# Kernel tuning notes

Measured on AMD Instinct MI355X. Metric: run time of the kernel, lower is better.

Reference implementation:

```python
import jax, jax.numpy as jnp
import numpy as np

SIZES = [(200000, 100000), (100000, 50000), (50000, 25000)]  # (n_src, n_dst) per layer
E = [1600000, 800000, 400000]
IN_C, HID, OUT_C = 128, 256, 47
BN_EPS = 1e-5


def setup_inputs() -> dict:
    key = jax.random.key(0)
    ks = jax.random.split(key, 32)
    inp = {"x": jax.random.normal(ks[0], (SIZES[0][0], IN_C), jnp.float32)}
    for i in range(3):
        inp[f"row{i}"] = jax.random.randint(ks[1 + 2 * i], (E[i],), 0, SIZES[i][0], dtype=jnp.int32)
        inp[f"col{i}"] = jax.random.randint(ks[2 + 2 * i], (E[i],), 0, SIZES[i][1], dtype=jnp.int32)
    dims = [IN_C, HID, HID]
    for i in range(3):
        inp[f"Wl{i}"] = jax.random.normal(ks[10 + 4 * i], (HID, dims[i]), jnp.float32) * 0.05
        inp[f"Wr{i}"] = jax.random.normal(ks[11 + 4 * i], (HID, dims[i]), jnp.float32) * 0.05
        inp[f"g{i}"] = jnp.ones((HID,), jnp.float32)
        inp[f"b{i}"] = jnp.zeros((HID,), jnp.float32)
    inp["Wlin"] = jax.random.normal(ks[25], (OUT_C, 3 * HID), jnp.float32) * 0.05
    inp["blin"] = jnp.zeros((OUT_C,), jnp.float32)
    return inp


def _sage_bn_relu(x_src, row, col, Wl, Wr, g, b, n_dst):
    """Bipartite SAGEConv (mean aggr, bias=False) + BatchNorm(eval) + ReLU."""
    x_dst = x_src[:n_dst]
    msg = x_src[row]                                             # [E, d] gather
    agg = jax.ops.segment_sum(msg, col, num_segments=n_dst)      # scatter-add
    cnt = jax.ops.segment_sum(jnp.ones(row.shape, x_src.dtype), col, num_segments=n_dst)
    agg = agg / jnp.maximum(cnt, 1.0)[:, None]                   # mean over in-neighbors
    h = agg @ Wl.T + x_dst @ Wr.T                                # lin_l + lin_r
    # BatchNorm1d in eval mode with fresh running stats (mean=0, var=1)
    h = h * jax.lax.rsqrt(jnp.asarray(1.0 + BN_EPS, h.dtype)) * g + b
    return jax.nn.relu(h)


def reference(x, row0, col0, row1, col1, row2, col2,
              Wl0, Wr0, g0, b0, Wl1, Wr1, g1, b1, Wl2, Wr2, g2, b2,
              Wlin, blin):
    rows = (row0, row1, row2)
    cols = (col0, col1, col2)
    Wls, Wrs = (Wl0, Wl1, Wl2), (Wr0, Wr1, Wr2)
    gs, bs = (g0, g1, g2), (b0, b1, b2)
    end = SIZES[-1][1]  # end_size = adj_t[-1][-1][1]
    h = x
    xs = []
    for i in range(3):
        h = _sage_bn_relu(h, rows[i], cols[i], Wls[i], Wrs[i], gs[i], bs[i], SIZES[i][1])
        xs.append(h[:end])
    z = jnp.concatenate(xs, axis=-1) @ Wlin.T + blin  # JK 'cat' + final Linear
    return jax.nn.log_softmax(z, axis=-1)
```

## Files before the change

### kernel.cpp

```cpp
#include <hip/hip_runtime.h>
#include <hip/hip_bf16.h>


#define N_DST0 100000
#define N_DST1 50000
#define N_DST2 25000
#define HID 256
#define OUTC 47
#define ENDR 25000
#define DRC 512
#define NBMAX 256
#define CHUNK 8192
#define BN_SCALE 0.99999500003749969f

#define SEL3(y, a, b, c) ((y) == 0 ? (a) : ((y) == 1 ? (b) : (c)))

typedef __attribute__((ext_vector_type(8))) short short8;
typedef __attribute__((ext_vector_type(4))) float f32x4;

__device__ __forceinline__ unsigned short f2b1(float f) {
    unsigned int u = __float_as_uint(f);
    return (unsigned short)((u + 0x7fffu + ((u >> 16) & 1u)) >> 16);
}
__device__ __forceinline__ float b2f_lo(unsigned int v) {
    return __uint_as_float(v << 16);
}
__device__ __forceinline__ float b2f_hi(unsigned int v) {
    return __uint_as_float(v & 0xffff0000u);
}
__device__ __forceinline__ unsigned int pack2(float lo, float hi) {
    return (unsigned int)f2b1(lo) | ((unsigned int)f2b1(hi) << 16);
}

__global__ __launch_bounds__(256) void f2b_kernel(
    const float* __restrict__ in, unsigned short* __restrict__ out, int n)
{
    int i = (blockIdx.x * 256 + threadIdx.x) * 4;
    if (i < n) {
        float4 v = *(const float4*)&in[i];
        uint2 o;
        o.x = pack2(v.x, v.y);
        o.y = pack2(v.z, v.w);
        *(uint2*)&out[i] = o;
    }
}

__global__ __launch_bounds__(256) void f2b_multi(
    const float* s0, const float* s1, const float* s2, const float* s3,
    const float* s4, const float* s5, const float* s6,
    unsigned short* d0, unsigned short* d1, unsigned short* d2,
    unsigned short* d3, unsigned short* d4, unsigned short* d5,
    unsigned short* d6)
{
    int idx = (blockIdx.x * 256 + threadIdx.x) * 4;
    const float* s; unsigned short* d; int off;
    if (idx < 65536)       { if (idx < 32768)  { s = s0; d = d0; off = 0; }
                             else              { s = s1; d = d1; off = 32768; } }
    else if (idx < 196608) { if (idx < 131072) { s = s2; d = d2; off = 65536; }
                             else              { s = s3; d = d3; off = 131072; } }
    else if (idx < 327680) { if (idx < 262144) { s = s4; d = d4; off = 196608; }
                             else              { s = s5; d = d5; off = 262144; } }
    else if (idx < 363776) { s = s6; d = d6; off = 327680; }
    else return;
    int j = idx - off;
    float4 v = *(const float4*)&s[j];
    uint2 o;
    o.x = pack2(v.x, v.y);
    o.y = pack2(v.z, v.w);
    *(uint2*)&d[j] = o;
}

__global__ __launch_bounds__(256) void bucket_hist_all(
    const int* c0, const int* c1, const int* c2,
    int* __restrict__ bhist, int E0, int E1, int E2)
{
    const int y = blockIdx.y;
    const int* col = SEL3(y, c0, c1, c2);
    const int E = SEL3(y, E0, E1, E2);
    __shared__ int h[NBMAX];
    const int t = threadIdx.x;
    h[t] = 0;
    __syncthreads();
    const int stride = gridDim.x * 256;
    for (int i = blockIdx.x * 256 + t; i < E; i += stride)
        atomicAdd(&h[col[i] >> 9], 1);
    __syncthreads();
    int v = h[t];
    if (v) atomicAdd(&bhist[(y * NBMAX + t) * 16], v);
}

__global__ __launch_bounds__(256) void bucket_scan_all(
    const int* __restrict__ bhist, int* __restrict__ bstart,
    int* __restrict__ bcur)
{
    const int y = blockIdx.x;
    const int t = threadIdx.x;
    __shared__ int sh[256];
    int v = bhist[(y * NBMAX + t) * 16];
    sh[t] = v;
    __syncthreads();
    for (int off = 1; off < 256; off <<= 1) {
        int x = (t >= off) ? sh[t - off] : 0;
        __syncthreads();
        sh[t] += x;
        __syncthreads();
    }
    int ex = sh[t] - v;
    bstart[y * (NBMAX + 1) + t] = ex;
    if (t == 255) bstart[y * (NBMAX + 1) + 256] = sh[255];
    bcur[y * NBMAX * 16 + t * 16] = ex;
}

__global__ __launch_bounds__(256) void multisplit_all(
    const int* r0, const int* r1, const int* r2,
    const int* c0, const int* c1, const int* c2,
    int* bcur, unsigned int* p0, unsigned int* p1, unsigned int* p2,
    int E0, int E1, int E2)
{
    const int y = blockIdx.y;
    const int E = SEL3(y, E0, E1, E2);
    const int base = blockIdx.x * CHUNK;
    if (base >= E) return;
    const int* row = SEL3(y, r0, r1, r2);
    const int* col = SEL3(y, c0, c1, c2);
    int* bc = bcur + y * (NBMAX * 16);
    unsigned int* part = SEL3(y, p0, p1, p2);

    __shared__ int hist[NBMAX];
    __shared__ int segoff[NBMAX + 1];
    __shared__ int cur[NBMAX];
    __shared__ int delta[NBMAX];
    __shared__ unsigned int stage[CHUNK];
    __shared__ unsigned char bstage[CHUNK];

    const int t = threadIdx.x;
    const int n = min(CHUNK, E - base);

    hist[t] = 0;
    __syncthreads();
    for (int i = t; i < n; i += 256)
        atomicAdd(&hist[col[base + i] >> 9], 1);
    __syncthreads();

    int v = hist[t];
    cur[t] = v;
    __syncthreads();
    for (int off = 1; off < 256; off <<= 1) {
        int x = (t >= off) ? cur[t - off] : 0;
        __syncthreads();
        cur[t] += x;
        __syncthreads();
    }
    segoff[t + 1] = cur[t];
    if (t == 0) segoff[0] = 0;
    __syncthreads();
    int so = segoff[t];
    cur[t] = so;
    if (v > 0) {
        int g = atomicAdd(&bc[t * 16], v);
        delta[t] = g - so;
    }
    __syncthreads();

    for (int i = t; i < n; i += 256) {
        int c = col[base + i];
        int r = row[base + i];
        int b = c >> 9;
        int p = atomicAdd(&cur[b], 1);
        stage[p] = ((unsigned)(c & 511) << 18) | (unsigned)r;
        bstage[p] = (unsigned char)b;
    }
    __syncthreads();

    for (int i = t; i < n; i += 256) {
        int b = bstage[i];
        part[delta[b] + i] = stage[i];
    }
}

__global__ __launch_bounds__(256) void bucket_csr_all(
    const unsigned int* p0, const unsigned int* p1, const unsigned int* p2,
    const int* __restrict__ bstart,
    int* g0, int* g1, int* g2, int* x0, int* x1, int* x2,
    int* s0, int* s1, int* s2, int n0, int n1, int n2)
{
    const int y = blockIdx.y;
    const int n_dst = SEL3(y, n0, n1, n2);
    const int b = blockIdx.x;
    const int d0 = b * DRC;
    if (d0 >= n_dst) return;
    const unsigned int* part = SEL3(y, p0, p1, p2);
    const int* bs = bstart + y * (NBMAX + 1);
    int* deg  = SEL3(y, g0, g1, g2);
    int* excl = SEL3(y, x0, x1, x2);
    int* esrc = SEL3(y, s0, s1, s2);

    __shared__ int h[DRC];
    __shared__ int cur2[DRC];
    __shared__ int tsum[256];
    const int t = threadIdx.x;
    h[t] = 0; h[t + 256] = 0;
    __syncthreads();
    const int wstart = bs[b], wend = bs[b + 1];
    for (int i = wstart + t; i < wend; i += 256)
        atomicAdd(&h[part[i] >> 18], 1);
    __syncthreads();

    int h0 = h[2 * t], h1 = h[2 * t + 1];
    int ps = h0 + h1;
    tsum[t] = ps;
    __syncthreads();
    for (int off = 1; off < 256; off <<= 1) {
        int x = (t >= off) ? tsum[t - off] : 0;
        __syncthreads();
        tsum[t] += x;
        __syncthreads();
    }
    int exp_ = tsum[t] - ps;
    cur2[2 * t]     = wstart + exp_;
    cur2[2 * t + 1] = wstart + exp_ + h0;
    __syncthreads();

    for (int j = t; j < DRC; j += 256) {
        int d = d0 + j;
        if (d < n_dst) { deg[d] = h[j]; excl[d] = cur2[j]; }
    }
    __syncthreads();

    for (int i = wstart + t; i < wend; i += 256) {
        unsigned int v = part[i];
        int pos = atomicAdd(&cur2[v >> 18], 1);
        esrc[pos] = (int)(v & 0x3FFFFu);
    }
}

template<int LOGK>
__global__ __launch_bounds__(256) void gather_mean(
    const unsigned short* __restrict__ xsrc, const int* __restrict__ esrc,
    const int* __restrict__ start, const int* __restrict__ deg,
    unsigned short* __restrict__ agg, int n_dst)
{
    const int wid = (blockIdx.x * 256 + threadIdx.x) >> 6;
    const int lane = threadIdx.x & 63;
    if (wid >= n_dst) return;
    const int sub = lane >> 5;
    const int cl  = lane & 31;
    const int s = start[wid];
    const int d = deg[wid];
    const float inv = 1.0f / (float)max(d, 1);

    if (LOGK == 7) {
        float a0 = 0, a1 = 0, a2 = 0, a3 = 0;
        const size_t coff = (size_t)cl * 4;
        int i = 0;
        for (; i + 8 <= d; i += 8) {
            int e0 = esrc[s + i + 0 + sub], e1 = esrc[s + i + 2 + sub];
            int e2 = esrc[s + i + 4 + sub], e3 = esrc[s + i + 6 + sub];
            uint2 v0 = *(const uint2*)&xsrc[((size_t)e0 << 7) + coff];
            uint2 v1 = *(const uint2*)&xsrc[((size_t)e1 << 7) + coff];
            uint2 v2 = *(const uint2*)&xsrc[((size_t)e2 << 7) + coff];
            uint2 v3 = *(const uint2*)&xsrc[((size_t)e3 << 7) + coff];
            a0 += b2f_lo(v0.x) + b2f_lo(v1.x) + b2f_lo(v2.x) + b2f_lo(v3.x);
            a1 += b2f_hi(v0.x) + b2f_hi(v1.x) + b2f_hi(v2.x) + b2f_hi(v3.x);
            a2 += b2f_lo(v0.y) + b2f_lo(v1.y) + b2f_lo(v2.y) + b2f_lo(v3.y);
            a3 += b2f_hi(v0.y) + b2f_hi(v1.y) + b2f_hi(v2.y) + b2f_hi(v3.y);
        }
        for (; i + 2 <= d; i += 2) {
            int e0 = esrc[s + i + sub];
            uint2 v0 = *(const uint2*)&xsrc[((size_t)e0 << 7) + coff];
            a0 += b2f_lo(v0.x); a1 += b2f_hi(v0.x);
            a2 += b2f_lo(v0.y); a3 += b2f_hi(v0.y);
        }
        if (i < d && sub == 0) {
            int e0 = esrc[s + i];
            uint2 v0 = *(const uint2*)&xsrc[((size_t)e0 << 7) + coff];
            a0 += b2f_lo(v0.x); a1 += b2f_hi(v0.x);
            a2 += b2f_lo(v0.y); a3 += b2f_hi(v0.y);
        }
        a0 += __shfl_xor(a0, 32); a1 += __shfl_xor(a1, 32);
        a2 += __shfl_xor(a2, 32); a3 += __shfl_xor(a3, 32);
        if (sub == 0) {
            uint2 o;
            o.x = pack2(a0 * inv, a1 * inv);
            o.y = pack2(a2 * inv, a3 * inv);
            *(uint2*)&agg[((size_t)wid << 7) + coff] = o;
        }
    } else {
        float a0 = 0, a1 = 0, a2 = 0, a3 = 0, a4 = 0, a5 = 0, a6 = 0, a7 = 0;
        const size_t coff = (size_t)cl * 8;
        int i = 0;
        for (; i + 8 <= d; i += 8) {
            int e0 = esrc[s + i + 0 + sub], e1 = esrc[s + i + 2 + sub];
            int e2 = esrc[s + i + 4 + sub], e3 = esrc[s + i + 6 + sub];
            uint4 v0 = *(const uint4*)&xsrc[((size_t)e0 << 8) + coff];
            uint4 v1 = *(const uint4*)&xsrc[((size_t)e1 << 8) + coff];
            uint4 v2 = *(const uint4*)&xsrc[((size_t)e2 << 8) + coff];
            uint4 v3 = *(const uint4*)&xsrc[((size_t)e3 << 8) + coff];
            a0 += b2f_lo(v0.x) + b2f_lo(v1.x) + b2f_lo(v2.x) + b2f_lo(v3.x);
            a1 += b2f_hi(v0.x) + b2f_hi(v1.x) + b2f_hi(v2.x) + b2f_hi(v3.x);
            a2 += b2f_lo(v0.y) + b2f_lo(v1.y) + b2f_lo(v2.y) + b2f_lo(v3.y);
            a3 += b2f_hi(v0.y) + b2f_hi(v1.y) + b2f_hi(v2.y) + b2f_hi(v3.y);
            a4 += b2f_lo(v0.z) + b2f_lo(v1.z) + b2f_lo(v2.z) + b2f_lo(v3.z);
            a5 += b2f_hi(v0.z) + b2f_hi(v1.z) + b2f_hi(v2.z) + b2f_hi(v3.z);
            a6 += b2f_lo(v0.w) + b2f_lo(v1.w) + b2f_lo(v2.w) + b2f_lo(v3.w);
            a7 += b2f_hi(v0.w) + b2f_hi(v1.w) + b2f_hi(v2.w) + b2f_hi(v3.w);
        }
        for (; i + 2 <= d; i += 2) {
            int e0 = esrc[s + i + sub];
            uint4 v0 = *(const uint4*)&xsrc[((size_t)e0 << 8) + coff];
            a0 += b2f_lo(v0.x); a1 += b2f_hi(v0.x);
            a2 += b2f_lo(v0.y); a3 += b2f_hi(v0.y);
            a4 += b2f_lo(v0.z); a5 += b2f_hi(v0.z);
            a6 += b2f_lo(v0.w); a7 += b2f_hi(v0.w);
        }
        if (i < d && sub == 0) {
            int e0 = esrc[s + i];
            uint4 v0 = *(const uint4*)&xsrc[((size_t)e0 << 8) + coff];
            a0 += b2f_lo(v0.x); a1 += b2f_hi(v0.x);
            a2 += b2f_lo(v0.y); a3 += b2f_hi(v0.y);
            a4 += b2f_lo(v0.z); a5 += b2f_hi(v0.z);
            a6 += b2f_lo(v0.w); a7 += b2f_hi(v0.w);
        }
        a0 += __shfl_xor(a0, 32); a1 += __shfl_xor(a1, 32);
        a2 += __shfl_xor(a2, 32); a3 += __shfl_xor(a3, 32);
        a4 += __shfl_xor(a4, 32); a5 += __shfl_xor(a5, 32);
        a6 += __shfl_xor(a6, 32); a7 += __shfl_xor(a7, 32);
        if (sub == 0) {
            uint4 o;
            o.x = pack2(a0 * inv, a1 * inv);
            o.y = pack2(a2 * inv, a3 * inv);
            o.z = pack2(a4 * inv, a5 * inv);
            o.w = pack2(a6 * inv, a7 * inv);
            *(uint4*)&agg[((size_t)wid << 8) + coff] = o;
        }
    }
}

template<int KH>
__global__ __launch_bounds__(512) void sage_gemm_mfma(
    const unsigned short* __restrict__ aggb, const unsigned short* __restrict__ xdstb,
    const unsigned short* __restrict__ Wlb, const unsigned short* __restrict__ Wrb,
    const float* __restrict__ g, const float* __restrict__ b,
    unsigned short* __restrict__ h, int n_dst)
{
    __shared__ uint4 A_sh[512];
    __shared__ uint4 B_sh[1024];

    const int tid  = threadIdx.x;
    const int lane = tid & 63;
    const int wv   = tid >> 6;
    const int mh   = wv >> 2;
    const int n0   = (wv & 3) * 64;
    const int m0g  = blockIdx.x * 128;
    const int lrow = lane & 15;
    const int lgrp = lane >> 4;

    f32x4 acc[4][4];
#pragma unroll
    for (int i = 0; i < 4; ++i)
#pragma unroll
        for (int j = 0; j < 4; ++j)
            acc[i][j] = (f32x4){0.f, 0.f, 0.f, 0.f};

    for (int kp = 0; kp < 2 * KH; kp += 32) {
        const unsigned short* Asrc = (kp < KH) ? aggb : xdstb;
        const unsigned short* Bsrc = (kp < KH) ? Wlb : Wrb;
        const int kbase = (kp < KH) ? kp : kp - KH;

        {
            int m = tid >> 2, gq = tid & 3;
            int r = m0g + m;
            uint4 v = {0, 0, 0, 0};
            if (r < n_dst) v = *(const uint4*)&Asrc[(size_t)r * KH + kbase + gq * 8];
            A_sh[m * 4 + (gq ^ ((m >> 1) & 3))] = v;
        }
        {
            int nb_ = tid >> 2, gq = tid & 3;
#pragma unroll
            for (int i2 = 0; i2 < 2; ++i2) {
                int n = nb_ + 128 * i2;
                uint4 v = *(const uint4*)&Bsrc[(size_t)n * KH + kbase + gq * 8];
                B_sh[n * 4 + (gq ^ ((n >> 1) & 3))] = v;
            }
        }
        __syncthreads();

        short8 av[4], bv[4];
#pragma unroll
        for (int mf = 0; mf < 4; ++mf) {
            int m = mh * 64 + mf * 16 + lrow;
            av[mf] = *reinterpret_cast<const short8*>(&A_sh[m * 4 + (lgrp ^ ((m >> 1) & 3))]);
        }
#pragma unroll
        for (int nf = 0; nf < 4; ++nf) {
            int n = n0 + nf * 16 + lrow;
            bv[nf] = *reinterpret_cast<const short8*>(&B_sh[n * 4 + (lgrp ^ ((n >> 1) & 3))]);
        }
#pragma unroll
        for (int mf = 0; mf < 4; ++mf)
#pragma unroll
            for (int nf = 0; nf < 4; ++nf)
                acc[mf][nf] = __builtin_amdgcn_mfma_f32_16x16x32_bf16(
                    av[mf], bv[nf], acc[mf][nf], 0, 0, 0);
        __syncthreads();
    }

#pragma unroll
    for (int nf = 0; nf < 4; ++nf) {
        int n = n0 + nf * 16 + lrow;
        float sc = g[n] * BN_SCALE;
        float bi = b[n];
#pragma unroll
        for (int mf = 0; mf < 4; ++mf) {
            int mbase = m0g + mh * 64 + mf * 16 + lgrp * 4;
#pragma unroll
            for (int r = 0; r < 4; ++r) {
                int m = mbase + r;
                if (m < n_dst) {
                    float vv = fmaxf(acc[mf][nf][r] * sc + bi, 0.f);
                    h[(size_t)m * HID + n] = f2b1(vv);
                }
            }
        }
    }
}

__global__ __launch_bounds__(256) void final_mfma(
    const unsigned short* __restrict__ h0, const unsigned short* __restrict__ h1,
    const unsigned short* __restrict__ h2, const unsigned short* __restrict__ wlinb,
    const float* __restrict__ blin, float* __restrict__ out)
{
    __shared__ uint4 A_sh[512];
    __shared__ uint4 B_sh[256];

    const int tid  = threadIdx.x;
    const int lane = tid & 63;
    const int wv   = tid >> 6;
    const int m0g  = blockIdx.x * 128;
    const int lrow = lane & 15;
    const int lgrp = lane >> 4;

    f32x4 acc[2][4];
#pragma unroll
    for (int i = 0; i < 2; ++i)
#pragma unroll
        for (int j = 0; j < 4; ++j)
            acc[i][j] = (f32x4){0.f, 0.f, 0.f, 0.f};

    for (int kp = 0; kp < 768; kp += 32) {
        const int seg = kp >> 8;
        const unsigned short* hs = (seg == 0) ? h0 : (seg == 1) ? h1 : h2;
        const int kseg = kp & 255;

#pragma unroll
        for (int l = 0; l < 2; ++l) {
            int idx = tid + l * 256;
            int m = idx >> 2, gq = idx & 3;
            int r = m0g + m;
            uint4 v = {0, 0, 0, 0};
            if (r < ENDR) v = *(const uint4*)&hs[(size_t)r * HID + kseg + gq * 8];
            A_sh[m * 4 + (gq ^ ((m >> 1) & 3))] = v;
        }
        {
            int n = tid >> 2, gq = tid & 3;
            uint4 v = *(const uint4*)&wlinb[(size_t)n * 768 + kp + gq * 8];
            B_sh[n * 4 + (gq ^ ((n >> 1) & 3))] = v;
        }
        __syncthreads();

        short8 av[2], bv[4];
#pragma unroll
        for (int mf = 0; mf < 2; ++mf) {
            int m = wv * 32 + mf * 16 + lrow;
            av[mf] = *reinterpret_cast<const short8*>(&A_sh[m * 4 + (lgrp ^ ((m >> 1) & 3))]);
        }
#pragma unroll
        for (int nf = 0; nf < 4; ++nf) {
            int n = nf * 16 + lrow;
            bv[nf] = *reinterpret_cast<const short8*>(&B_sh[n * 4 + (lgrp ^ ((n >> 1) & 3))]);
        }
#pragma unroll
        for (int mf = 0; mf < 2; ++mf)
#pragma unroll
            for (int nf = 0; nf < 4; ++nf)
                acc[mf][nf] = __builtin_amdgcn_mfma_f32_16x16x32_bf16(
                    av[mf], bv[nf], acc[mf][nf], 0, 0, 0);
        __syncthreads();
    }

    float bv4[4];
#pragma unroll
    for (int nf = 0; nf < 4; ++nf) {
        int n = nf * 16 + lrow;
        bv4[nf] = (n < OUTC) ? blin[n] : 0.f;
    }

#pragma unroll
    for (int mf = 0; mf < 2; ++mf) {
        float z[4][4];
        float rmax[4], rsum[4];
#pragma unroll
        for (int r = 0; r < 4; ++r) {
            float mx = -INFINITY;
#pragma unroll
            for (int nf = 0; nf < 4; ++nf) {
                int n = nf * 16 + lrow;
                float v = (n < OUTC) ? acc[mf][nf][r] + bv4[nf] : -INFINITY;
                z[r][nf] = v;
                mx = fmaxf(mx, v);
            }
            rmax[r] = mx;
        }
#pragma unroll
        for (int off = 8; off >= 1; off >>= 1)
#pragma unroll
            for (int r = 0; r < 4; ++r)
                rmax[r] = fmaxf(rmax[r], __shfl_xor(rmax[r], off));
#pragma unroll
        for (int r = 0; r < 4; ++r) {
            float s = 0.f;
#pragma unroll
            for (int nf = 0; nf < 4; ++nf)
                s += (z[r][nf] > -INFINITY) ? expf(z[r][nf] - rmax[r]) : 0.f;
            rsum[r] = s;
        }
#pragma unroll
        for (int off = 8; off >= 1; off >>= 1)
#pragma unroll
            for (int r = 0; r < 4; ++r)
                rsum[r] += __shfl_xor(rsum[r], off);

#pragma unroll
        for (int r = 0; r < 4; ++r) {
            int m = m0g + wv * 32 + mf * 16 + lgrp * 4 + r;
            if (m < ENDR) {
                float lg = rmax[r] + logf(rsum[r]);
#pragma unroll
                for (int nf = 0; nf < 4; ++nf) {
                    int n = nf * 16 + lrow;
                    if (n < OUTC) out[(size_t)m * OUTC + n] = z[r][nf] - lg;
                }
            }
        }
    }
}

extern "C" void kernel_launch(void* const* d_in, const int* in_sizes, int n_in,
                              void* d_out, int out_size, void* d_ws, size_t ws_size,
                              hipStream_t stream)
{
    const float* x    = (const float*)d_in[0];
    const int* rows[3] = {(const int*)d_in[1], (const int*)d_in[3], (const int*)d_in[5]};
    const int* cols[3] = {(const int*)d_in[2], (const int*)d_in[4], (const int*)d_in[6]};
    const float* Wl[3] = {(const float*)d_in[7],  (const float*)d_in[11], (const float*)d_in[15]};
    const float* Wr[3] = {(const float*)d_in[8],  (const float*)d_in[12], (const float*)d_in[16]};
    const float* gs[3] = {(const float*)d_in[9],  (const float*)d_in[13], (const float*)d_in[17]};
    const float* bs[3] = {(const float*)d_in[10], (const float*)d_in[14], (const float*)d_in[18]};
    const float* Wlin = (const float*)d_in[19];
    const float* blin = (const float*)d_in[20];
    float* out = (float*)d_out;

    const int E0 = in_sizes[1], E1 = in_sizes[3], E2 = in_sizes[5];

    char* base = (char*)d_ws;
    unsigned short* xb   = (unsigned short*)(base);
    unsigned short* h0b  = (unsigned short*)(base + 51200000);
    unsigned short* h1b  = (unsigned short*)(base + 102400000);
    unsigned short* h2b  = (unsigned short*)(base + 128000000);
    unsigned short* aggb = (unsigned short*)(base + 140800000);
    unsigned short* wb   = (unsigned short*)(base + 166400000);
    unsigned short* wlinb= (unsigned short*)(base + 167100032);
    int* ibase = (int*)(base + 167600000);
    int* esrc0 = ibase;
    int* esrc1 = ibase + 1600000;
    int* esrc2 = ibase + 2400000;
    int* deg0  = ibase + 2800000;
    int* deg1  = ibase + 2900000;
    int* deg2  = ibase + 2950000;
    int* excl0 = ibase + 3000000;
    int* excl1 = ibase + 3100000;
    int* excl2 = ibase + 3150000;
    int* bcur  = ibase + 3200000;
    int* bhist = ibase + 3220000;
    int* bstart= ibase + 3240000;
    unsigned int* part0 = (unsigned int*)(base + 181000000);
    unsigned int* part1 = (unsigned int*)(base + 188000000);
    unsigned int* part2 = (unsigned int*)(base + 192000000);

    unsigned short* Wlb[3] = {wb,          wb + 65536,  wb + 196608};
    unsigned short* Wrb[3] = {wb + 32768,  wb + 131072, wb + 262144};

    f2b_kernel<<<(25600000 / 4 + 255) / 256, 256, 0, stream>>>(x, xb, 25600000);
    hipMemsetAsync(wlinb, 0, 64 * 768 * sizeof(unsigned short), stream);
    f2b_multi<<<356, 256, 0, stream>>>(
        Wl[0], Wr[0], Wl[1], Wr[1], Wl[2], Wr[2], Wlin,
        Wlb[0], Wrb[0], Wlb[1], Wrb[1], Wlb[2], Wrb[2], wlinb);

    hipMemsetAsync(bhist, 0, 3 * NBMAX * 16 * sizeof(int), stream);
    {
        dim3 gh(128, 3);
        bucket_hist_all<<<gh, 256, 0, stream>>>(
            cols[0], cols[1], cols[2], bhist, E0, E1, E2);
        bucket_scan_all<<<3, 256, 0, stream>>>(bhist, bstart, bcur);
        dim3 gms((E0 + CHUNK - 1) / CHUNK, 3);
        multisplit_all<<<gms, 256, 0, stream>>>(
            rows[0], rows[1], rows[2], cols[0], cols[1], cols[2],
            bcur, part0, part1, part2, E0, E1, E2);
        dim3 gbc((N_DST0 + DRC - 1) / DRC, 3);
        bucket_csr_all<<<gbc, 256, 0, stream>>>(
            part0, part1, part2, bstart,
            deg0, deg1, deg2, excl0, excl1, excl2,
            esrc0, esrc1, esrc2, N_DST0, N_DST1, N_DST2);
    }

    const unsigned short* hsrc[3] = {xb, h0b, h1b};
    unsigned short* hdst[3] = {h0b, h1b, h2b};
    int* esrcs[3] = {esrc0, esrc1, esrc2};
    int* excls[3] = {excl0, excl1, excl2};
    int* degs[3]  = {deg0, deg1, deg2};
    const int ndst[3] = {N_DST0, N_DST1, N_DST2};

    for (int L = 0; L < 3; ++L) {
        const int nd = ndst[L];
        if (L == 0) {
            gather_mean<7><<<(nd + 3) / 4, 256, 0, stream>>>(
                hsrc[L], esrcs[L], excls[L], degs[L], aggb, nd);
            sage_gemm_mfma<128><<<(nd + 127) / 128, 512, 0, stream>>>(
                aggb, hsrc[L], Wlb[L], Wrb[L], gs[L], bs[L], hdst[L], nd);
        } else {
            gather_mean<8><<<(nd + 3) / 4, 256, 0, stream>>>(
                hsrc[L], esrcs[L], excls[L], degs[L], aggb, nd);
            sage_gemm_mfma<256><<<(nd + 127) / 128, 512, 0, stream>>>(
                aggb, hsrc[L], Wlb[L], Wrb[L], gs[L], bs[L], hdst[L], nd);
        }
    }

    final_mfma<<<(ENDR + 127) / 128, 256, 0, stream>>>(
        h0b, h1b, h2b, wlinb, blin, out);
}
```

Baseline: 406.1 us.

## Switch intermediates to fp16 with packed-half gather and LDS-staged GEMM epilogue

Replaces bf16 storage and MFMA with fp16 throughout, which lets the gather accumulate with packed half-precision vector adds instead of per-element bf16-to-float unpacking. The layer-0 gather now uses 16-byte loads with four edge groups per wave. The GEMM epilogue stages the output tile in shared memory so rows are written to global memory as coalesced 16-byte stores instead of scattered 2-byte stores. Accumulating in fp16 risks precision loss and overflow for high-degree nodes.

Result: faster. 372.9 us (-8.2%).

```diff
diff --git a/kernel.cpp b/kernel.cpp
--- a/kernel.cpp
+++ b/kernel.cpp
@@ -15,45 +15,37 @@
 
 #define SEL3(y, a, b, c) ((y) == 0 ? (a) : ((y) == 1 ? (b) : (c)))
 
-typedef __attribute__((ext_vector_type(8))) short short8;
+typedef _Float16 f16x8 __attribute__((ext_vector_type(8)));
+typedef _Float16 f16x4 __attribute__((ext_vector_type(4)));
 typedef __attribute__((ext_vector_type(4))) float f32x4;
 
-__device__ __forceinline__ unsigned short f2b1(float f) {
-    unsigned int u = __float_as_uint(f);
-    return (unsigned short)((u + 0x7fffu + ((u >> 16) & 1u)) >> 16);
-}
-__device__ __forceinline__ float b2f_lo(unsigned int v) {
-    return __uint_as_float(v << 16);
-}
-__device__ __forceinline__ float b2f_hi(unsigned int v) {
-    return __uint_as_float(v & 0xffff0000u);
-}
-__device__ __forceinline__ unsigned int pack2(float lo, float hi) {
-    return (unsigned int)f2b1(lo) | ((unsigned int)f2b1(hi) << 16);
-}
-
-__global__ __launch_bounds__(256) void f2b_kernel(
-    const float* __restrict__ in, unsigned short* __restrict__ out, int n)
+__device__ __forceinline__ f16x8 hshfl_add(f16x8 a, int m) {
+    union { f16x8 h; int i[4]; } u, v;
+    u.h = a;
+#pragma unroll
+    for (int j = 0; j < 4; ++j) v.i[j] = __shfl_xor(u.i[j], m);
+    return a + v.h;
+}
+
+__global__ __launch_bounds__(256) void f2h_kernel(
+    const float* __restrict__ in, _Float16* __restrict__ out, int n)
 {
     int i = (blockIdx.x * 256 + threadIdx.x) * 4;
     if (i < n) {
         float4 v = *(const float4*)&in[i];
-        uint2 o;
-        o.x = pack2(v.x, v.y);
-        o.y = pack2(v.z, v.w);
-        *(uint2*)&out[i] = o;
-    }
-}
-
-__global__ __launch_bounds__(256) void f2b_multi(
+        f16x4 o = {(_Float16)v.x, (_Float16)v.y, (_Float16)v.z, (_Float16)v.w};
+        *(f16x4*)&out[i] = o;
+    }
+}
+
+__global__ __launch_bounds__(256) void f2h_multi(
     const float* s0, const float* s1, const float* s2, const float* s3,
     const float* s4, const float* s5, const float* s6,
-    unsigned short* d0, unsigned short* d1, unsigned short* d2,
-    unsigned short* d3, unsigned short* d4, unsigned short* d5,
-    unsigned short* d6)
+    _Float16* d0, _Float16* d1, _Float16* d2, _Float16* d3,
+    _Float16* d4, _Float16* d5, _Float16* d6)
 {
     int idx = (blockIdx.x * 256 + threadIdx.x) * 4;
-    const float* s; unsigned short* d; int off;
+    const float* s; _Float16* d; int off;
     if (idx < 65536)       { if (idx < 32768)  { s = s0; d = d0; off = 0; }
                              else              { s = s1; d = d1; off = 32768; } }
     else if (idx < 196608) { if (idx < 131072) { s = s2; d = d2; off = 65536; }
@@ -64,10 +56,8 @@
     else return;
     int j = idx - off;
     float4 v = *(const float4*)&s[j];
-    uint2 o;
-    o.x = pack2(v.x, v.y);
-    o.y = pack2(v.z, v.w);
-    *(uint2*)&d[j] = o;
+    f16x4 o = {(_Float16)v.x, (_Float16)v.y, (_Float16)v.z, (_Float16)v.w};
+    *(f16x4*)&d[j] = o;
 }
 
 __global__ __launch_bounds__(256) void bucket_hist_all(
@@ -236,115 +226,88 @@
 
 template<int LOGK>
 __global__ __launch_bounds__(256) void gather_mean(
-    const unsigned short* __restrict__ xsrc, const int* __restrict__ esrc,
+    const _Float16* __restrict__ xsrc, const int* __restrict__ esrc,
     const int* __restrict__ start, const int* __restrict__ deg,
-    unsigned short* __restrict__ agg, int n_dst)
+    _Float16* __restrict__ agg, int n_dst)
 {
     const int wid = (blockIdx.x * 256 + threadIdx.x) >> 6;
     const int lane = threadIdx.x & 63;
     if (wid >= n_dst) return;
-    const int sub = lane >> 5;
-    const int cl  = lane & 31;
     const int s = start[wid];
     const int d = deg[wid];
     const float inv = 1.0f / (float)max(d, 1);
+    f16x8 acc = {0, 0, 0, 0, 0, 0, 0, 0};
 
     if (LOGK == 7) {
-        float a0 = 0, a1 = 0, a2 = 0, a3 = 0;
-        const size_t coff = (size_t)cl * 4;
-        int i = 0;
-        for (; i + 8 <= d; i += 8) {
-            int e0 = esrc[s + i + 0 + sub], e1 = esrc[s + i + 2 + sub];
-            int e2 = esrc[s + i + 4 + sub], e3 = esrc[s + i + 6 + sub];
-            uint2 v0 = *(const uint2*)&xsrc[((size_t)e0 << 7) + coff];
-            uint2 v1 = *(const uint2*)&xsrc[((size_t)e1 << 7) + coff];
-            uint2 v2 = *(const uint2*)&xsrc[((size_t)e2 << 7) + coff];
-            uint2 v3 = *(const uint2*)&xsrc[((size_t)e3 << 7) + coff];
-            a0 += b2f_lo(v0.x) + b2f_lo(v1.x) + b2f_lo(v2.x) + b2f_lo(v3.x);
-            a1 += b2f_hi(v0.x) + b2f_hi(v1.x) + b2f_hi(v2.x) + b2f_hi(v3.x);
-            a2 += b2f_lo(v0.y) + b2f_lo(v1.y) + b2f_lo(v2.y) + b2f_lo(v3.y);
-            a3 += b2f_hi(v0.y) + b2f_hi(v1.y) + b2f_hi(v2.y) + b2f_hi(v3.y);
-        }
-        for (; i + 2 <= d; i += 2) {
-            int e0 = esrc[s + i + sub];
-            uint2 v0 = *(const uint2*)&xsrc[((size_t)e0 << 7) + coff];
-            a0 += b2f_lo(v0.x); a1 += b2f_hi(v0.x);
-            a2 += b2f_lo(v0.y); a3 += b2f_hi(v0.y);
-        }
-        if (i < d && sub == 0) {
-            int e0 = esrc[s + i];
-            uint2 v0 = *(const uint2*)&xsrc[((size_t)e0 << 7) + coff];
-            a0 += b2f_lo(v0.x); a1 += b2f_hi(v0.x);
-            a2 += b2f_lo(v0.y); a3 += b2f_hi(v0.y);
-        }
-        a0 += __shfl_xor(a0, 32); a1 += __shfl_xor(a1, 32);
-        a2 += __shfl_xor(a2, 32); a3 += __shfl_xor(a3, 32);
-        if (sub == 0) {
-            uint2 o;
-            o.x = pack2(a0 * inv, a1 * inv);
-            o.y = pack2(a2 * inv, a3 * inv);
-            *(uint2*)&agg[((size_t)wid << 7) + coff] = o;
-        }
-    } else {
-        float a0 = 0, a1 = 0, a2 = 0, a3 = 0, a4 = 0, a5 = 0, a6 = 0, a7 = 0;
+        const int sub = lane >> 4;
+        const int cl  = lane & 15;
         const size_t coff = (size_t)cl * 8;
         int i = 0;
         for (; i + 8 <= d; i += 8) {
-            int e0 = esrc[s + i + 0 + sub], e1 = esrc[s + i + 2 + sub];
+            int e0 = esrc[s + i + sub], e1 = esrc[s + i + 4 + sub];
+            f16x8 v0 = *(const f16x8*)&xsrc[((size_t)e0 << 7) + coff];
+            f16x8 v1 = *(const f16x8*)&xsrc[((size_t)e1 << 7) + coff];
+            acc += v0;
+            acc += v1;
+        }
+        for (; i + 4 <= d; i += 4) {
+            int e0 = esrc[s + i + sub];
+            acc += *(const f16x8*)&xsrc[((size_t)e0 << 7) + coff];
+        }
+        if (i + sub < d) {
+            int e0 = esrc[s + i + sub];
+            acc += *(const f16x8*)&xsrc[((size_t)e0 << 7) + coff];
+        }
+        acc = hshfl_add(acc, 16);
+        acc = hshfl_add(acc, 32);
+        if (sub == 0) {
+            f16x8 o;
+#pragma unroll
+            for (int j = 0; j < 8; ++j) o[j] = (_Float16)((float)acc[j] * inv);
+            *(f16x8*)&agg[((size_t)wid << 7) + coff] = o;
+        }
+    } else {
+        const int sub = lane >> 5;
+        const int cl  = lane & 31;
+        const size_t coff = (size_t)cl * 8;
+        int i = 0;
+        for (; i + 8 <= d; i += 8) {
+            int e0 = esrc[s + i + sub],     e1 = esrc[s + i + 2 + sub];
             int e2 = esrc[s + i + 4 + sub], e3 = esrc[s + i + 6 + sub];
-            uint4 v0 = *(const uint4*)&xsrc[((size_t)e0 << 8) + coff];
-            uint4 v1 = *(const uint4*)&xsrc[((size_t)e1 << 8) + coff];
-            uint4 v2 = *(const uint4*)&xsrc[((size_t)e2 << 8) + coff];
-            uint4 v3 = *(const uint4*)&xsrc[((size_t)e3 << 8) + coff];
-            a0 += b2f_lo(v0.x) + b2f_lo(v1.x) + b2f_lo(v2.x) + b2f_lo(v3.x);
-            a1 += b2f_hi(v0.x) + b2f_hi(v1.x) + b2f_hi(v2.x) + b2f_hi(v3.x);
-            a2 += b2f_lo(v0.y) + b2f_lo(v1.y) + b2f_lo(v2.y) + b2f_lo(v3.y);
-            a3 += b2f_hi(v0.y) + b2f_hi(v1.y) + b2f_hi(v2.y) + b2f_hi(v3.y);
-            a4 += b2f_lo(v0.z) + b2f_lo(v1.z) + b2f_lo(v2.z) + b2f_lo(v3.z);
-            a5 += b2f_hi(v0.z) + b2f_hi(v1.z) + b2f_hi(v2.z) + b2f_hi(v3.z);
-            a6 += b2f_lo(v0.w) + b2f_lo(v1.w) + b2f_lo(v2.w) + b2f_lo(v3.w);
-            a7 += b2f_hi(v0.w) + b2f_hi(v1.w) + b2f_hi(v2.w) + b2f_hi(v3.w);
+            f16x8 v0 = *(const f16x8*)&xsrc[((size_t)e0 << 8) + coff];
+            f16x8 v1 = *(const f16x8*)&xsrc[((size_t)e1 << 8) + coff];
+            f16x8 v2 = *(const f16x8*)&xsrc[((size_t)e2 << 8) + coff];
+            f16x8 v3 = *(const f16x8*)&xsrc[((size_t)e3 << 8) + coff];
+            acc += v0; acc += v1; acc += v2; acc += v3;
         }
         for (; i + 2 <= d; i += 2) {
             int e0 = esrc[s + i + sub];
-            uint4 v0 = *(const uint4*)&xsrc[((size_t)e0 << 8) + coff];
-            a0 += b2f_lo(v0.x); a1 += b2f_hi(v0.x);
-            a2 += b2f_lo(v0.y); a3 += b2f_hi(v0.y);
-            a4 += b2f_lo(v0.z); a5 += b2f_hi(v0.z);
-            a6 += b2f_lo(v0.w); a7 += b2f_hi(v0.w);
-        }
-        if (i < d && sub == 0) {
-            int e0 = esrc[s + i];
-            uint4 v0 = *(const uint4*)&xsrc[((size_t)e0 << 8) + coff];
-            a0 += b2f_lo(v0.x); a1 += b2f_hi(v0.x);
-            a2 += b2f_lo(v0.y); a3 += b2f_hi(v0.y);
-            a4 += b2f_lo(v0.z); a5 += b2f_hi(v0.z);
-            a6 += b2f_lo(v0.w); a7 += b2f_hi(v0.w);
-        }
-        a0 += __shfl_xor(a0, 32); a1 += __shfl_xor(a1, 32);
-        a2 += __shfl_xor(a2, 32); a3 += __shfl_xor(a3, 32);
-        a4 += __shfl_xor(a4, 32); a5 += __shfl_xor(a5, 32);
-        a6 += __shfl_xor(a6, 32); a7 += __shfl_xor(a7, 32);
+            acc += *(const f16x8*)&xsrc[((size_t)e0 << 8) + coff];
+        }
+        if (i + sub < d) {
+            int e0 = esrc[s + i + sub];
+            acc += *(const f16x8*)&xsrc[((size_t)e0 << 8) + coff];
+        }
+        acc = hshfl_add(acc, 32);
         if (sub == 0) {
-            uint4 o;
-            o.x = pack2(a0 * inv, a1 * inv);
-            o.y = pack2(a2 * inv, a3 * inv);
-            o.z = pack2(a4 * inv, a5 * inv);
-            o.w = pack2(a6 * inv, a7 * inv);
-            *(uint4*)&agg[((size_t)wid << 8) + coff] = o;
+            f16x8 o;
+#pragma unroll
+            for (int j = 0; j < 8; ++j) o[j] = (_Float16)((float)acc[j] * inv);
+            *(f16x8*)&agg[((size_t)wid << 8) + coff] = o;
         }
     }
 }
 
 template<int KH>
 __global__ __launch_bounds__(512) void sage_gemm_mfma(
-    const unsigned short* __restrict__ aggb, const unsigned short* __restrict__ xdstb,
-    const unsigned short* __restrict__ Wlb, const unsigned short* __restrict__ Wrb,
+    const _Float16* __restrict__ aggb, const _Float16* __restrict__ xdstb,
+    const _Float16* __restrict__ Wlb, const _Float16* __restrict__ Wrb,
     const float* __restrict__ g, const float* __restrict__ b,
-    unsigned short* __restrict__ h, int n_dst)
-{
-    __shared__ uint4 A_sh[512];
-    __shared__ uint4 B_sh[1024];
+    _Float16* __restrict__ h, int n_dst)
+{
+    __shared__ uint4 SH[2176];
+    uint4* A_sh = SH;
+    uint4* B_sh = SH + 512;
 
     const int tid  = threadIdx.x;
     const int lane = tid & 63;
@@ -363,8 +326,8 @@
             acc[i][j] = (f32x4){0.f, 0.f, 0.f, 0.f};
 
     for (int kp = 0; kp < 2 * KH; kp += 32) {
-        const unsigned short* Asrc = (kp < KH) ? aggb : xdstb;
-        const unsigned short* Bsrc = (kp < KH) ? Wlb : Wrb;
+        const _Float16* Asrc = (kp < KH) ? aggb : xdstb;
+        const _Float16* Bsrc = (kp < KH) ? Wlb : Wrb;
         const int kbase = (kp < KH) ? kp : kp - KH;
 
         {
@@ -385,49 +348,65 @@
         }
         __syncthreads();
 
-        short8 av[4], bv[4];
+        f16x8 av[4], bv[4];
 #pragma unroll
         for (int mf = 0; mf < 4; ++mf) {
             int m = mh * 64 + mf * 16 + lrow;
-            av[mf] = *reinterpret_cast<const short8*>(&A_sh[m * 4 + (lgrp ^ ((m >> 1) & 3))]);
+            av[mf] = *reinterpret_cast<const f16x8*>(&A_sh[m * 4 + (lgrp ^ ((m >> 1) & 3))]);
         }
 #pragma unroll
         for (int nf = 0; nf < 4; ++nf) {
             int n = n0 + nf * 16 + lrow;
-            bv[nf] = *reinterpret_cast<const short8*>(&B_sh[n * 4 + (lgrp ^ ((n >> 1) & 3))]);
+            bv[nf] = *reinterpret_cast<const f16x8*>(&B_sh[n * 4 + (lgrp ^ ((n >> 1) & 3))]);
         }
 #pragma unroll
         for (int mf = 0; mf < 4; ++mf)
 #pragma unroll
             for (int nf = 0; nf < 4; ++nf)
-                acc[mf][nf] = __builtin_amdgcn_mfma_f32_16x16x32_bf16(
+                acc[mf][nf] = __builtin_amdgcn_mfma_f32_16x16x32_f16(
                     av[mf], bv[nf], acc[mf][nf], 0, 0, 0);
         __syncthreads();
     }
 
-#pragma unroll
-    for (int nf = 0; nf < 4; ++nf) {
-        int n = n0 + nf * 16 + lrow;
-        float sc = g[n] * BN_SCALE;
-        float bi = b[n];
-#pragma unroll
-        for (int mf = 0; mf < 4; ++mf) {
-            int mbase = m0g + mh * 64 + mf * 16 + lgrp * 4;
-#pragma unroll
-            for (int r = 0; r < 4; ++r) {
-                int m = mbase + r;
-                if (m < n_dst) {
-                    float vv = fmaxf(acc[mf][nf][r] * sc + bi, 0.f);
-                    h[(size_t)m * HID + n] = f2b1(vv);
+    unsigned short* C_sh = (unsigned short*)SH;
+#pragma unroll
+    for (int half = 0; half < 2; ++half) {
+        __syncthreads();
+        if (mh == half) {
+#pragma unroll
+            for (int nf = 0; nf < 4; ++nf) {
+                int n = n0 + nf * 16 + lrow;
+                float sc = g[n] * BN_SCALE;
+                float bi = b[n];
+#pragma unroll
+                for (int mf = 0; mf < 4; ++mf) {
+                    int mloc = mf * 16 + lgrp * 4;
+#pragma unroll
+                    for (int r = 0; r < 4; ++r) {
+                        float vv = fmaxf(acc[mf][nf][r] * sc + bi, 0.f);
+                        _Float16 hv = (_Float16)vv;
+                        C_sh[(mloc + r) * 264 + n] = *(unsigned short*)&hv;
+                    }
                 }
             }
         }
+        __syncthreads();
+        int mbase = m0g + half * 64;
+#pragma unroll
+        for (int k = 0; k < 4; ++k) {
+            int idx = tid + k * 512;
+            int rr = idx >> 5, cc = idx & 31;
+            int m = mbase + rr;
+            if (m < n_dst)
+                *(uint4*)&h[(size_t)m * HID + cc * 8] =
+                    *(const uint4*)&C_sh[rr * 264 + cc * 8];
+        }
     }
 }
 
 __global__ __launch_bounds__(256) void final_mfma(
-    const unsigned short* __restrict__ h0, const unsigned short* __restrict__ h1,
-    const unsigned short* __restrict__ h2, const unsigned short* __restrict__ wlinb,
+    const _Float16* __restrict__ h0, const _Float16* __restrict__ h1,
+    const _Float16* __restrict__ h2, const _Float16* __restrict__ wlinb,
     const float* __restrict__ blin, float* __restrict__ out)
 {
     __shared__ uint4 A_sh[512];
@@ -449,7 +428,7 @@
 
     for (int kp = 0; kp < 768; kp += 32) {
         const int seg = kp >> 8;
-        const unsigned short* hs = (seg == 0) ? h0 : (seg == 1) ? h1 : h2;
+        const _Float16* hs = (seg == 0) ? h0 : (seg == 1) ? h1 : h2;
         const int kseg = kp & 255;
 
 #pragma unroll
@@ -468,22 +447,22 @@
         }
         __syncthreads();
 
-        short8 av[2], bv[4];
+        f16x8 av[2], bv[4];
 #pragma unroll
         for (int mf = 0; mf < 2; ++mf) {
             int m = wv * 32 + mf * 16 + lrow;
-            av[mf] = *reinterpret_cast<const short8*>(&A_sh[m * 4 + (lgrp ^ ((m >> 1) & 3))]);
+            av[mf] = *reinterpret_cast<const f16x8*>(&A_sh[m * 4 + (lgrp ^ ((m >> 1) & 3))]);
         }
 #pragma unroll
         for (int nf = 0; nf < 4; ++nf) {
             int n = nf * 16 + lrow;
-            bv[nf] = *reinterpret_cast<const short8*>(&B_sh[n * 4 + (lgrp ^ ((n >> 1) & 3))]);
+            bv[nf] = *reinterpret_cast<const f16x8*>(&B_sh[n * 4 + (lgrp ^ ((n >> 1) & 3))]);
         }
 #pragma unroll
         for (int mf = 0; mf < 2; ++mf)
 #pragma unroll
             for (int nf = 0; nf < 4; ++nf)
-                acc[mf][nf] = __builtin_amdgcn_mfma_f32_16x16x32_bf16(
+                acc[mf][nf] = __builtin_amdgcn_mfma_f32_16x16x32_f16(
                     av[mf], bv[nf], acc[mf][nf], 0, 0, 0);
         __syncthreads();
     }
@@ -563,13 +542,13 @@
     const int E0 = in_sizes[1], E1 = in_sizes[3], E2 = in_sizes[5];
 
     char* base = (char*)d_ws;
-    unsigned short* xb   = (unsigned short*)(base);
-    unsigned short* h0b  = (unsigned short*)(base + 51200000);
-    unsigned short* h1b  = (unsigned short*)(base + 102400000);
-    unsigned short* h2b  = (unsigned short*)(base + 128000000);
-    unsigned short* aggb = (unsigned short*)(base + 140800000);
-    unsigned short* wb   = (unsigned short*)(base + 166400000);
-    unsigned short* wlinb= (unsigned short*)(base + 167100032);
+    _Float16* xb   = (_Float16*)(base);
+    _Float16* h0b  = (_Float16*)(base + 51200000);
+    _Float16* h1b  = (_Float16*)(base + 102400000);
+    _Float16* h2b  = (_Float16*)(base + 128000000);
+    _Float16* aggb = (_Float16*)(base + 140800000);
+    _Float16* wb   = (_Float16*)(base + 166400000);
+    _Float16* wlinb= (_Float16*)(base + 167100032);
     int* ibase = (int*)(base + 167600000);
     int* esrc0 = ibase;
     int* esrc1 = ibase + 1600000;
@@ -587,12 +566,12 @@
     unsigned int* part1 = (unsigned int*)(base + 188000000);
     unsigned int* part2 = (unsigned int*)(base + 192000000);
 
-    unsigned short* Wlb[3] = {wb,          wb + 65536,  wb + 196608};
-    unsigned short* Wrb[3] = {wb + 32768,  wb + 131072, wb + 262144};
-
-    f2b_kernel<<<(25600000 / 4 + 255) / 256, 256, 0, stream>>>(x, xb, 25600000);
-    hipMemsetAsync(wlinb, 0, 64 * 768 * sizeof(unsigned short), stream);
-    f2b_multi<<<356, 256, 0, stream>>>(
+    _Float16* Wlb[3] = {wb,          wb + 65536,  wb + 196608};
+    _Float16* Wrb[3] = {wb + 32768,  wb + 131072, wb + 262144};
+
+    f2h_kernel<<<(25600000 / 4 + 255) / 256, 256, 0, stream>>>(x, xb, 25600000);
+    hipMemsetAsync(wlinb, 0, 64 * 768 * sizeof(_Float16), stream);
+    f2h_multi<<<356, 256, 0, stream>>>(
         Wl[0], Wr[0], Wl[1], Wr[1], Wl[2], Wr[2], Wlin,
         Wlb[0], Wrb[0], Wlb[1], Wrb[1], Wlb[2], Wrb[2], wlinb);
 
@@ -613,8 +592,8 @@
             esrc0, esrc1, esrc2, N_DST0, N_DST1, N_DST2);
     }
 
-    const unsigned short* hsrc[3] = {xb, h0b, h1b};
-    unsigned short* hdst[3] = {h0b, h1b, h2b};
+    const _Float16* hsrc[3] = {xb, h0b, h1b};
+    _Float16* hdst[3] = {h0b, h1b, h2b};
     int* esrcs[3] = {esrc0, esrc1, esrc2};
     int* excls[3] = {excl0, excl1, excl2};
     int* degs[3]  = {deg0, deg1, deg2};
```
